# Kernel optimization log

Measured on AMD Instinct MI355X. Metric: run time of the kernel, lower is better.

## Reference

```python
import jax, jax.numpy as jnp
import numpy as np

N_QUBITS = 11
N_LAYERS = 4
N_FEATURES = 8
N_SAMPLES = 16
MEAS_QUBITS = (0, 1, 2, 3)
DIM = 2 ** N_QUBITS


def _cnot_matrix(control, target, n):
    # Faithful to get_single_CNOT_matrix: qubit 0 is the MOST significant bit
    # (bin(i).zfill(n) indexing). Column i maps to row with target bit flipped
    # when control bit is 1.
    idx = np.arange(2 ** n)
    ctrl = (idx >> (n - 1 - control)) & 1
    rows = np.where(ctrl == 1, idx ^ (1 << (n - 1 - target)), idx)
    u = np.zeros((2 ** n, 2 ** n), np.float32)
    u[rows, idx] = 1.0
    return jnp.asarray(u, jnp.complex64)


def _get_angles(X, weights, biases):
    # X: (B, F) -> angles (B, L, Q, 3), tiling features with repetition
    B, F = X.shape
    n_angles = N_QUBITS * N_LAYERS * 3
    reps = n_angles // F + 1
    Xe = jnp.tile(X, (1, reps))[:, :n_angles].reshape(B, N_LAYERS, N_QUBITS, 3)
    return Xe * weights[None] + biases[None]


def _single_qubit_unitaries(ang):
    # ang: (B, Q, 3) = (phi, theta, omega)  ->  (B, Q, 2, 2) complex Rot gates
    phi, theta, omega = ang[..., 0], ang[..., 1], ang[..., 2]
    ct = jnp.cos(theta / 2)
    st = jnp.sin(theta / 2)
    po = (phi + omega) / 2
    pm = (phi - omega) / 2
    m00 = jnp.exp(-1j * po) * ct
    m01 = -jnp.exp(1j * pm) * st
    m10 = jnp.exp(-1j * pm) * st
    m11 = jnp.exp(1j * po) * ct
    M = jnp.stack([m00, m01, m10, m11], axis=-1)
    return M.reshape(ang.shape[0], ang.shape[1], 2, 2).astype(jnp.complex64)


def _system_unitary(M):
    # Sequential Kronecker product over qubits (qubit 0 = leftmost factor),
    # identical math to the source's einsum-based kron: (B, 2^n, 2^n).
    B = M.shape[0]
    U = M[:, 0]
    for q in range(1, N_QUBITS):
        d = U.shape[1]
        U = (U[:, :, None, :, None] * M[:, q][:, None, :, None, :]).reshape(B, d * 2, d * 2)
    return U


def setup_inputs() -> dict:
    key = jax.random.key(0)
    k1, k2, k3 = jax.random.split(key, 3)
    X = jax.random.normal(k1, (N_SAMPLES, N_FEATURES), jnp.float32)
    weights = jax.random.uniform(k2, (N_LAYERS, N_QUBITS, 3), jnp.float32)
    biases = jax.random.uniform(k3, (N_LAYERS, N_QUBITS, 3), jnp.float32)
    return {"X": X, "weights": weights, "biases": biases}


def reference(X, weights, biases):
    B = X.shape[0]
    angles = _get_angles(X, weights, biases)  # (B, L, Q, 3)
    state = jnp.zeros((B, DIM), jnp.complex64).at[:, 0].set(1.0)
    ring = [(i, i + 1) for i in range(N_QUBITS - 1)] + [(N_QUBITS - 1, 0)]
    cnots = [_cnot_matrix(c, t, N_QUBITS) for c, t in ring]
    for l in range(N_LAYERS):
        U = _system_unitary(_single_qubit_unitaries(angles[:, l]))  # (B, D, D)
        state = jnp.einsum('aij,aj->ai', U, state)
        for Uc in cnots:
            state = jnp.einsum('ij,aj->ai', Uc, state)
    probs = jnp.abs(state) ** 2  # (B, D) float32
    idx = jnp.arange(DIM)
    outs = [jnp.sum(probs * (1.0 - 2.0 * ((idx >> (N_QUBITS - 1 - q)) & 1)).astype(probs.dtype), axis=1)
            for q in MEAS_QUBITS]
    return jnp.stack(outs, axis=1)  # (B, n_meas)
```

## Files before the change

kernel.cpp:

```cpp
#include <hip/hip_runtime.h>

#define NQ 11
#define NL 4
#define NF 8
#define DIM 2048
#define NGATES (NL * NQ)

__device__ __forceinline__ int ring_perm(int y) {
    int z = y ^ ((y & 1) << 10);
#pragma unroll
    for (int k = 10; k >= 1; --k) {
        z ^= ((z >> (11 - k)) & 1) << (10 - k);
    }
    return z;
}

__global__ __launch_bounds__(1024)
void qsim_kernel(const float* __restrict__ X, const float* __restrict__ W,
                 const float* __restrict__ Bi, float* __restrict__ out)
{
    __shared__ float2 bufA[DIM];
    __shared__ float2 bufB[DIM];
    __shared__ float gm[NGATES][8];
    __shared__ float red[16][4];

    const int b = blockIdx.x;
    const int t = threadIdx.x;

    float2* cur = bufA;
    float2* nxt = bufB;

    cur[t]        = make_float2(0.f, 0.f);
    cur[t + 1024] = make_float2(0.f, 0.f);
    if (t == 0) cur[0] = make_float2(1.f, 0.f);

    if (t < NGATES) {
        const int base = t * 3;
        const float x0 = X[b * NF + ((base + 0) & 7)];
        const float x1 = X[b * NF + ((base + 1) & 7)];
        const float x2 = X[b * NF + ((base + 2) & 7)];
        const float phi   = x0 * W[base + 0] + Bi[base + 0];
        const float theta = x1 * W[base + 1] + Bi[base + 1];
        const float omega = x2 * W[base + 2] + Bi[base + 2];

        float sh, ch;   sincosf(0.5f * theta, &sh, &ch);
        float spo, cpo; sincosf(0.5f * (phi + omega), &spo, &cpo);
        float spm, cpm; sincosf(0.5f * (phi - omega), &spm, &cpm);
        gm[t][0] =  cpo * ch;  gm[t][1] = -spo * ch;
        gm[t][2] = -cpm * sh;  gm[t][3] = -spm * sh;
        gm[t][4] =  cpm * sh;  gm[t][5] = -spm * sh;
        gm[t][6] =  cpo * ch;  gm[t][7] =  spo * ch;
    }
    __syncthreads();

    for (int l = 0; l < NL; ++l) {
#pragma unroll
        for (int q = 0; q < NQ; ++q) {
            const int g = l * NQ + q;
            const float4* gmv = (const float4*)gm[g];
            const float4 M0 = gmv[0];
            const float4 M1 = gmv[1];

            const int p  = 10 - q;
            const int m  = 1 << p;
            const int i0 = ((t >> p) << (p + 1)) | (t & (m - 1));
            const int i1 = i0 | m;

            const float2 a = cur[i0];
            const float2 c = cur[i1];
            float2 na, nc;
            na.x = M0.x * a.x - M0.y * a.y + M0.z * c.x - M0.w * c.y;
            na.y = M0.x * a.y + M0.y * a.x + M0.z * c.y + M0.w * c.x;
            nc.x = M1.x * a.x - M1.y * a.y + M1.z * c.x - M1.w * c.y;
            nc.y = M1.x * a.y + M1.y * a.x + M1.z * c.y + M1.w * c.x;
            cur[i0] = na;
            cur[i1] = nc;
            __syncthreads();
        }
        nxt[t]        = cur[ring_perm(t)];
        nxt[t + 1024] = cur[ring_perm(t + 1024)];
        __syncthreads();
        float2* tmp = cur; cur = nxt; nxt = tmp;
    }

    float v[4];
    {
        const int iA = t, iB = t + 1024;
        const float2 a = cur[iA];
        const float2 c = cur[iB];
        const float pa = a.x * a.x + a.y * a.y;
        const float pc = c.x * c.x + c.y * c.y;
#pragma unroll
        for (int k = 0; k < 4; ++k) {
            const int pos = 10 - k;
            const float sa = 1.f - 2.f * (float)((iA >> pos) & 1);
            const float sc = 1.f - 2.f * (float)((iB >> pos) & 1);
            v[k] = sa * pa + sc * pc;
        }
    }
#pragma unroll
    for (int k = 0; k < 4; ++k) {
#pragma unroll
        for (int off = 32; off >= 1; off >>= 1)
            v[k] += __shfl_down(v[k], off, 64);
    }
    const int lane = t & 63;
    const int wave = t >> 6;
    if (lane == 0) {
#pragma unroll
        for (int k = 0; k < 4; ++k) red[wave][k] = v[k];
    }
    __syncthreads();
    if (t < 4) {
        float s = 0.f;
#pragma unroll
        for (int w = 0; w < 16; ++w) s += red[w][t];
        out[b * 4 + t] = s;
    }
}

extern "C" void kernel_launch(void* const* d_in, const int* in_sizes, int n_in,
                              void* d_out, int out_size, void* d_ws, size_t ws_size,
                              hipStream_t stream) {
    const float* X  = (const float*)d_in[0];
    const float* W  = (const float*)d_in[1];
    const float* Bi = (const float*)d_in[2];
    float* out = (float*)d_out;
    qsim_kernel<<<16, 1024, 0, stream>>>(X, W, Bi, out);
}
```

Measured before the change: 72.05 us.

## Fuse gates into 3-qubit register groups and fold CNOT ring into loads

Each thread now holds 8 amplitudes in registers and applies three single-qubit gates per shared-memory pass, cutting barriers from 11+1 per layer to 4. The CNOT ring permutation is folded into the gather of the next layer's first group and into the final measurement. Shared-memory indices are XOR-swizzled to avoid bank conflicts, and the block shrinks from 1024 to 256 threads. The cost is more registers per thread and more complex index logic, with less thread-level parallelism per block.

Result: faster. 69.13 us (-4.1%).

```diff
diff --git a/kernel.cpp b/kernel.cpp
--- a/kernel.cpp
+++ b/kernel.cpp
@@ -6,33 +6,91 @@
 #define DIM 2048
 #define NGATES (NL * NQ)
 
-__device__ __forceinline__ int ring_perm(int y) {
+__host__ __device__ constexpr int ring_perm(int y) {
     int z = y ^ ((y & 1) << 10);
-#pragma unroll
-    for (int k = 10; k >= 1; --k) {
+    for (int k = 10; k >= 1; --k)
         z ^= ((z >> (11 - k)) & 1) << (10 - k);
-    }
     return z;
 }
 
-__global__ __launch_bounds__(1024)
+__device__ __forceinline__ int swz(int i) { return i ^ ((i >> 5) & 31); }
+
+__device__ __forceinline__ void rot_pair(float2& a, float2& c,
+                                         const float4 M0, const float4 M1) {
+    float2 na, nc;
+    na.x = M0.x * a.x - M0.y * a.y + M0.z * c.x - M0.w * c.y;
+    na.y = M0.x * a.y + M0.y * a.x + M0.z * c.y + M0.w * c.x;
+    nc.x = M1.x * a.x - M1.y * a.y + M1.z * c.x - M1.w * c.y;
+    nc.y = M1.x * a.y + M1.y * a.x + M1.z * c.y + M1.w * c.x;
+    a = na; c = nc;
+}
+
+template<int P2, int P1, int P0, bool PERM>
+__device__ __forceinline__ void group3(const float2* __restrict__ src,
+                                       float2* __restrict__ dst,
+                                       const float (*gm)[8], int g, int base) {
+    constexpr int E2 = 1 << P2, E1 = 1 << P1, E0 = 1 << P0;
+    constexpr int K2 = PERM ? ring_perm(1 << P2) : (1 << P2);
+    constexpr int K1 = PERM ? ring_perm(1 << P1) : (1 << P1);
+    constexpr int K0 = PERM ? ring_perm(1 << P0) : (1 << P0);
+
+    const float4* mA = (const float4*)gm[g];
+    const float4* mB = (const float4*)gm[g + 1];
+    const float4* mC = (const float4*)gm[g + 2];
+    const float4 A0 = mA[0], A1 = mA[1];
+    const float4 B0 = mB[0], B1 = mB[1];
+    const float4 C0 = mC[0], C1 = mC[1];
+
+    const int rb = PERM ? ring_perm(base) : base;
+    float2 s[8];
+#pragma unroll
+    for (int k = 0; k < 8; ++k) {
+        const int idx = rb ^ ((k & 4) ? K2 : 0) ^ ((k & 2) ? K1 : 0) ^ ((k & 1) ? K0 : 0);
+        s[k] = src[swz(idx)];
+    }
+    rot_pair(s[0], s[4], A0, A1); rot_pair(s[1], s[5], A0, A1);
+    rot_pair(s[2], s[6], A0, A1); rot_pair(s[3], s[7], A0, A1);
+    rot_pair(s[0], s[2], B0, B1); rot_pair(s[1], s[3], B0, B1);
+    rot_pair(s[4], s[6], B0, B1); rot_pair(s[5], s[7], B0, B1);
+    rot_pair(s[0], s[1], C0, C1); rot_pair(s[2], s[3], C0, C1);
+    rot_pair(s[4], s[5], C0, C1); rot_pair(s[6], s[7], C0, C1);
+#pragma unroll
+    for (int k = 0; k < 8; ++k) {
+        const int a = base | ((k & 4) ? E2 : 0) | ((k & 2) ? E1 : 0) | ((k & 1) ? E0 : 0);
+        dst[swz(a)] = s[k];
+    }
+}
+
+__device__ __forceinline__ void group2q(float2* buf, const float (*gm)[8],
+                                        int g, int t) {
+    const float4* mB = (const float4*)gm[g];
+    const float4* mC = (const float4*)gm[g + 1];
+    const float4 B0 = mB[0], B1 = mB[1];
+    const float4 C0 = mC[0], C1 = mC[1];
+#pragma unroll
+    for (int j = 0; j < 2; ++j) {
+        const int base = (t + 256 * j) << 2;
+        float2 s[4];
+#pragma unroll
+        for (int k = 0; k < 4; ++k) s[k] = buf[swz(base | k)];
+        rot_pair(s[0], s[2], B0, B1); rot_pair(s[1], s[3], B0, B1);
+        rot_pair(s[0], s[1], C0, C1); rot_pair(s[2], s[3], C0, C1);
+#pragma unroll
+        for (int k = 0; k < 4; ++k) buf[swz(base | k)] = s[k];
+    }
+}
+
+__global__ __launch_bounds__(256)
 void qsim_kernel(const float* __restrict__ X, const float* __restrict__ W,
                  const float* __restrict__ Bi, float* __restrict__ out)
 {
     __shared__ float2 bufA[DIM];
     __shared__ float2 bufB[DIM];
-    __shared__ float gm[NGATES][8];
-    __shared__ float red[16][4];
+    __shared__ __align__(16) float gm[NGATES][8];
+    __shared__ float red[4][4];
 
     const int b = blockIdx.x;
     const int t = threadIdx.x;
-
-    float2* cur = bufA;
-    float2* nxt = bufB;
-
-    cur[t]        = make_float2(0.f, 0.f);
-    cur[t + 1024] = make_float2(0.f, 0.f);
-    if (t == 0) cur[0] = make_float2(1.f, 0.f);
 
     if (t < NGATES) {
         const int base = t * 3;
@@ -42,7 +100,6 @@
         const float phi   = x0 * W[base + 0] + Bi[base + 0];
         const float theta = x1 * W[base + 1] + Bi[base + 1];
         const float omega = x2 * W[base + 2] + Bi[base + 2];
-
         float sh, ch;   sincosf(0.5f * theta, &sh, &ch);
         float spo, cpo; sincosf(0.5f * (phi + omega), &spo, &cpo);
         float spm, cpm; sincosf(0.5f * (phi - omega), &spm, &cpm);
@@ -51,71 +108,56 @@
         gm[t][4] =  cpm * sh;  gm[t][5] = -spm * sh;
         gm[t][6] =  cpo * ch;  gm[t][7] =  spo * ch;
     }
+#pragma unroll
+    for (int k = 0; k < 8; ++k) bufA[swz(t + 256 * k)] = make_float2(0.f, 0.f);
+    if (t == 0) bufA[0] = make_float2(1.f, 0.f);
     __syncthreads();
 
-    for (int l = 0; l < NL; ++l) {
-#pragma unroll
-        for (int q = 0; q < NQ; ++q) {
-            const int g = l * NQ + q;
-            const float4* gmv = (const float4*)gm[g];
-            const float4 M0 = gmv[0];
-            const float4 M1 = gmv[1];
+    float2* S = bufA;
+    float2* T = bufB;
+    const int base765 = ((t >> 5) << 8) | (t & 31);
+    const int base432 = ((t >> 2) << 5) | (t & 3);
 
-            const int p  = 10 - q;
-            const int m  = 1 << p;
-            const int i0 = ((t >> p) << (p + 1)) | (t & (m - 1));
-            const int i1 = i0 | m;
+    group3<10, 9, 8, false>(S, T, gm, 0, t); { float2* x = S; S = T; T = x; }
+    __syncthreads();
+    group3<7, 6, 5, false>(S, S, gm, 3, base765);  __syncthreads();
+    group3<4, 3, 2, false>(S, S, gm, 6, base432);  __syncthreads();
+    group2q(S, gm, 9, t);                          __syncthreads();
 
-            const float2 a = cur[i0];
-            const float2 c = cur[i1];
-            float2 na, nc;
-            na.x = M0.x * a.x - M0.y * a.y + M0.z * c.x - M0.w * c.y;
-            na.y = M0.x * a.y + M0.y * a.x + M0.z * c.y + M0.w * c.x;
-            nc.x = M1.x * a.x - M1.y * a.y + M1.z * c.x - M1.w * c.y;
-            nc.y = M1.x * a.y + M1.y * a.x + M1.z * c.y + M1.w * c.x;
-            cur[i0] = na;
-            cur[i1] = nc;
-            __syncthreads();
-        }
-        nxt[t]        = cur[ring_perm(t)];
-        nxt[t + 1024] = cur[ring_perm(t + 1024)];
+    for (int l = 1; l < NL; ++l) {
+        group3<10, 9, 8, true>(S, T, gm, l * NQ + 0, t); { float2* x = S; S = T; T = x; }
         __syncthreads();
-        float2* tmp = cur; cur = nxt; nxt = tmp;
+        group3<7, 6, 5, false>(S, S, gm, l * NQ + 3, base765);  __syncthreads();
+        group3<4, 3, 2, false>(S, S, gm, l * NQ + 6, base432);  __syncthreads();
+        group2q(S, gm, l * NQ + 9, t);                          __syncthreads();
     }
 
-    float v[4];
-    {
-        const int iA = t, iB = t + 1024;
-        const float2 a = cur[iA];
-        const float2 c = cur[iB];
-        const float pa = a.x * a.x + a.y * a.y;
-        const float pc = c.x * c.x + c.y * c.y;
+    const int rp_t = ring_perm(t);
+    float v[4] = {0.f, 0.f, 0.f, 0.f};
 #pragma unroll
-        for (int k = 0; k < 4; ++k) {
-            const int pos = 10 - k;
-            const float sa = 1.f - 2.f * (float)((iA >> pos) & 1);
-            const float sc = 1.f - 2.f * (float)((iB >> pos) & 1);
-            v[k] = sa * pa + sc * pc;
-        }
+    for (int k = 0; k < 8; ++k) {
+        const int src = rp_t ^ ((k & 4) ? ring_perm(1 << 10) : 0)
+                             ^ ((k & 2) ? ring_perm(1 << 9)  : 0)
+                             ^ ((k & 1) ? ring_perm(1 << 8)  : 0);
+        const float2 a = S[swz(src)];
+        const float p = a.x * a.x + a.y * a.y;
+        v[0] += (k & 4) ? -p : p;
+        v[1] += (k & 2) ? -p : p;
+        v[2] += (k & 1) ? -p : p;
+        v[3] += (t & 128) ? -p : p;
     }
 #pragma unroll
-    for (int k = 0; k < 4; ++k) {
+    for (int q = 0; q < 4; ++q)
 #pragma unroll
         for (int off = 32; off >= 1; off >>= 1)
-            v[k] += __shfl_down(v[k], off, 64);
-    }
-    const int lane = t & 63;
-    const int wave = t >> 6;
-    if (lane == 0) {
+            v[q] += __shfl_down(v[q], off, 64);
+    if ((t & 63) == 0) {
 #pragma unroll
-        for (int k = 0; k < 4; ++k) red[wave][k] = v[k];
+        for (int q = 0; q < 4; ++q) red[t >> 6][q] = v[q];
     }
     __syncthreads();
     if (t < 4) {
-        float s = 0.f;
-#pragma unroll
-        for (int w = 0; w < 16; ++w) s += red[w][t];
-        out[b * 4 + t] = s;
+        out[b * 4 + t] = red[0][t] + red[1][t] + red[2][t] + red[3][t];
     }
 }
 
@@ -126,5 +168,5 @@
     const float* W  = (const float*)d_in[1];
     const float* Bi = (const float*)d_in[2];
     float* out = (float*)d_out;
-    qsim_kernel<<<16, 1024, 0, stream>>>(X, W, Bi, out);
+    qsim_kernel<<<16, 256, 0, stream>>>(X, W, Bi, out);
 }
```
